# Kernel tuning notes

Measured on AMD Instinct MI355X. Metric: run time of the kernel, lower is better.

The kernel has to match this reference:

```python
import jax, jax.numpy as jnp
import numpy as np

R = 2
TAU = 0.1
EPS = 1e-7

# normalized 3x3 Sobel kernels (kornia SpatialGradient, normalized=True -> /8)
_GX = jnp.array([[-1., 0., 1.], [-2., 0., 2.], [-1., 0., 1.]], dtype=jnp.float32) / 8.0
_GY = _GX.T

K = 2 * R - 1  # 3
_HORIZ = jnp.zeros((K, K), jnp.float32).at[R - 1, :].set(1.0)
_VERT = jnp.zeros((K, K), jnp.float32).at[:, R - 1].set(1.0)
_LEAD = jnp.eye(K, dtype=jnp.float32)
_CNT = jnp.fliplr(jnp.eye(K, dtype=jnp.float32))


def _conv2d_same(x, k2d, mode):
    # depthwise 'same' cross-correlation, x: (B,C,H,W), k2d: (k,k)
    C = x.shape[1]
    p = k2d.shape[-1] // 2
    xp = jnp.pad(x, ((0, 0), (0, 0), (p, p), (p, p)), mode=mode)
    kern = jnp.broadcast_to(k2d[None, None], (C, 1) + k2d.shape)
    return jax.lax.conv_general_dilated(
        xp, kern, (1, 1), 'VALID',
        dimension_numbers=('NCHW', 'OIHW', 'NCHW'),
        feature_group_count=C)


def _grad_angles(t):
    # kornia SpatialGradient pads with replicate ('edge')
    gx = _conv2d_same(t, _GX, 'edge')
    gy = _conv2d_same(t, _GY, 'edge')
    grad_xx = _conv2d_same(gx, _GX, 'edge')
    grad_xy = _conv2d_same(gy, _GX, 'edge')
    grad_yy = _conv2d_same(gy, _GY, 'edge')
    theta = jnp.arctan(grad_yy * jnp.sign(-grad_xy + EPS) / (grad_xx + EPS))
    angle = theta * (180.0 / np.pi)
    return jnp.where(angle < 0, angle + 180.0, angle)


def _nms_loss(true_labels, pred_labels):
    angle = _grad_angles(true_labels)
    mask = (true_labels > 0).astype(jnp.float32)

    th_h = mask * (((angle >= 0) & (angle < 22.5)) | ((angle >= 157.5) & (angle < 180))).astype(jnp.float32)
    th_cd = mask * ((angle >= 22.5) & (angle < 67.5)).astype(jnp.float32)
    th_v = mask * ((angle >= 67.5) & (angle < 112.5)).astype(jnp.float32)
    th_ld = mask * ((angle > 112.5) & (angle < 157.5)).astype(jnp.float32)

    e = jnp.exp(pred_labels * TAU)

    def term(th, kern):
        f = _conv2d_same(e, kern, 'reflect')  # kornia filter2D default border 'reflect'
        return th * jnp.log(jnp.clip(e / (f + EPS), EPS, 1.0))

    total = (term(th_h, _HORIZ) + term(th_v, _VERT) +
             term(th_ld, _LEAD) + term(th_cd, _CNT))
    # sum over (C,H,W) per sample, mean over batch, negate
    return -jnp.mean(jnp.sum(total, axis=(1, 2, 3)))


def setup_inputs() -> dict:
    key = jax.random.key(0)
    k1, k2 = jax.random.split(key)
    B, C, H, W = 4, 19, 512, 512
    true_labels = jax.random.normal(k1, (B, C, H, W), dtype=jnp.float32)
    pred_labels = jax.random.normal(k2, (B, C, H, W), dtype=jnp.float32)
    return {"true_labels": true_labels, "pred_labels": pred_labels}


def reference(true_labels, pred_labels):
    return _nms_loss(true_labels, pred_labels)
```

## Files before the change

### kernel.cpp

```cpp
#include <hip/hip_runtime.h>

#define BAND 16
#define NITER (BAND + 4)
#define NSLOT 1024

__global__ __launch_bounds__(64) void nms_loss_kernel(
    const float* __restrict__ tl, const float* __restrict__ pl,
    double* __restrict__ acc_d, float* __restrict__ acc_f,
    int H, int W)
{
    const int y0   = blockIdx.x * BAND;
    const int slab = blockIdx.y;
    const int ch   = blockIdx.z;
    const float* tc = tl + (size_t)ch * H * W;
    const float* pc = pl + (size_t)ch * H * W;
    const int tid  = threadIdx.x;
    const int c0 = (slab << 7) + (tid << 1);
    const int oa = min(max(c0 - 2, 0), W - 2);
    const int oc = min(c0 + 2, W - 2);
    const bool xedge = (c0 == 0) || (c0 == W - 2);

    float P1h[5][2], P2h[5][2], P3h[5][2];
    float eh[3][4], tch[3][2];
    float tA[6], pA[6], tB[6], pB[6];

    #define LOADROW(I, T6, P6) {                                                   \
        int tr_ = y0 - 2 + (I); tr_ = min(max(tr_, 0), H - 1);                      \
        int pr_ = y0 - 3 + (I); pr_ = pr_ < 0 ? -pr_ : (pr_ >= H ? 2*H-2-pr_ : pr_);\
        const float* tb_ = tc + (size_t)tr_ * W;                                    \
        const float* pb_ = pc + (size_t)pr_ * W;                                    \
        float2 a_ = *(const float2*)(tb_ + oa), b_ = *(const float2*)(tb_ + c0),    \
               c_ = *(const float2*)(tb_ + oc);                                     \
        T6[0]=a_.x; T6[1]=a_.y; T6[2]=b_.x; T6[3]=b_.y; T6[4]=c_.x; T6[5]=c_.y;     \
        a_ = *(const float2*)(pb_ + oa); b_ = *(const float2*)(pb_ + c0);           \
        c_ = *(const float2*)(pb_ + oc);                                            \
        P6[0]=a_.x; P6[1]=a_.y; P6[2]=b_.x; P6[3]=b_.y; P6[4]=c_.x; P6[5]=c_.y; }

    #define CONSUME(T6, P6) {                                                       \
        if (!xedge) {                                                               \
            float s04 = T6[0] + T6[4], s13 = T6[1] + T6[3];                         \
            P1h[sP][0] = fmaf(-2.f, T6[2], s04);                                    \
            P3h[sP][0] = fmaf(6.f, T6[2], fmaf(4.f, s13, s04));                     \
            P2h[sP][0] = fmaf(2.f, T6[3] - T6[1], T6[4] - T6[0]);                   \
            float s04b = T6[1] + T6[5], s13b = T6[2] + T6[4];                       \
            P1h[sP][1] = fmaf(-2.f, T6[3], s04b);                                   \
            P3h[sP][1] = fmaf(6.f, T6[3], fmaf(4.f, s13b, s04b));                   \
            P2h[sP][1] = fmaf(2.f, T6[4] - T6[2], T6[5] - T6[1]);                   \
        } else if (c0 == 0) {                                                       \
            P1h[sP][0] = T6[4] - T6[3];                                             \
            P2h[sP][0] = fmaf(-2.f, T6[2], T6[3] + T6[4]);                          \
            P3h[sP][0] = fmaf(10.f, T6[2], fmaf(5.f, T6[3], T6[4]));                \
            P1h[sP][1] = fmaf(-2.f, T6[3], T6[2] + T6[5]);                          \
            P2h[sP][1] = fmaf(-3.f, T6[2], fmaf(2.f, T6[4], T6[5]));                \
            P3h[sP][1] = fmaf(5.f, T6[2], fmaf(6.f, T6[3], fmaf(4.f, T6[4], T6[5])));\
        } else {                                                                    \
            P1h[sP][0] = fmaf(-2.f, T6[2], T6[0] + T6[3]);                          \
            P2h[sP][0] = fmaf(3.f, T6[3], fmaf(-2.f, T6[1], -T6[0]));               \
            P3h[sP][0] = fmaf(5.f, T6[3], fmaf(6.f, T6[2], fmaf(4.f, T6[1], T6[0])));\
            P1h[sP][1] = T6[1] - T6[2];                                             \
            P2h[sP][1] = fmaf(2.f, T6[3], -T6[1] - T6[2]);                          \
            P3h[sP][1] = fmaf(10.f, T6[3], fmaf(5.f, T6[2], T6[1]));                \
        }                                                                           \
        tch[sE][0] = T6[2]; tch[sE][1] = T6[3];                                     \
        eh[sE][0] = __expf(0.1f * P6[1]);                                           \
        eh[sE][1] = __expf(0.1f * P6[2]);                                           \
        eh[sE][2] = __expf(0.1f * P6[3]);                                           \
        eh[sE][3] = __expf(0.1f * P6[4]); }

    LOADROW(0, tA, pA)
    LOADROW(1, tB, pB)

    float partial = 0.f;

    #pragma unroll
    for (int i = 0; i < NITER; ++i) {
        const int sP = i % 5, sE = i % 3;

        if ((i & 1) == 0) {
            CONSUME(tA, pA)
            if (i + 2 < NITER) LOADROW(i + 2, tA, pA)
        } else {
            CONSUME(tB, pB)
            if (i + 2 < NITER) LOADROW(i + 2, tB, pB)
        }

        if (i >= 4) {
            const int y = y0 + i - 4;
            const int s0 = (i - 4) % 5, s1 = (i - 3) % 5, s2 = (i - 2) % 5,
                      s3 = (i - 1) % 5, s4 = i % 5;
            float xx[2], xy[2], yy[2];
            if (y >= 2 && y <= H - 3) {
                #pragma unroll
                for (int j = 0; j < 2; ++j) {
                    float a04 = P1h[s0][j] + P1h[s4][j], a13 = P1h[s1][j] + P1h[s3][j];
                    xx[j] = fmaf(6.f, P1h[s2][j], fmaf(4.f, a13, a04));
                    xy[j] = fmaf(2.f, P2h[s3][j] - P2h[s1][j], P2h[s4][j] - P2h[s0][j]);
                    yy[j] = fmaf(-2.f, P3h[s2][j], P3h[s0][j] + P3h[s4][j]);
                }
            } else {
                float wss[5], wsd[5], wdd[5];
                if (y == 0) {
                    wss[0]=0; wss[1]=0; wss[2]=10; wss[3]=5;  wss[4]=1;
                    wsd[0]=0; wsd[1]=0; wsd[2]=-4; wsd[3]=3;  wsd[4]=1;
                    wdd[0]=0; wdd[1]=0; wdd[2]=0;  wdd[3]=-1; wdd[4]=1;
                } else if (y == 1) {
                    wss[0]=0; wss[1]=5; wss[2]=6;  wss[3]=4;  wss[4]=1;
                    wsd[0]=0; wsd[1]=-3;wsd[2]=0;  wsd[3]=2;  wsd[4]=1;
                    wdd[0]=0; wdd[1]=1; wdd[2]=-2; wdd[3]=0;  wdd[4]=1;
                } else if (y == H - 1) {
                    wss[0]=1; wss[1]=5; wss[2]=10; wss[3]=0;  wss[4]=0;
                    wsd[0]=-1;wsd[1]=-3;wsd[2]=4;  wsd[3]=0;  wsd[4]=0;
                    wdd[0]=1; wdd[1]=-1;wdd[2]=0;  wdd[3]=0;  wdd[4]=0;
                } else {
                    wss[0]=1; wss[1]=4; wss[2]=6;  wss[3]=5;  wss[4]=0;
                    wsd[0]=-1;wsd[1]=-2;wsd[2]=0;  wsd[3]=3;  wsd[4]=0;
                    wdd[0]=1; wdd[1]=0; wdd[2]=-2; wdd[3]=1;  wdd[4]=0;
                }
                const int ss[5] = {s0, s1, s2, s3, s4};
                #pragma unroll
                for (int j = 0; j < 2; ++j) {
                    float X = 0.f, Y = 0.f, Z = 0.f;
                    #pragma unroll
                    for (int k = 0; k < 5; ++k) {
                        X = fmaf(wss[k], P1h[ss[k]][j], X);
                        Y = fmaf(wsd[k], P2h[ss[k]][j], Y);
                        Z = fmaf(wdd[k], P3h[ss[k]][j], Z);
                    }
                    xx[j] = X; xy[j] = Y; yy[j] = Z;
                }
            }

            const int et = (i - 2) % 3, em = (i - 1) % 3, eb = i % 3;
            #pragma unroll
            for (int j = 0; j < 2; ++j) {
                if (tch[et][j] > 0.f) {
                    float den = xx[j] + 6.4e-6f;
                    float sa  = 6.4e-6f - xy[j];
                    float ax = fabsf(den), ay = fabsf(yy[j]);
                    bool isH = ay < 0.41421356f * ax;
                    bool isV = ay >= 2.41421356f * ax;
                    bool qp  = ((yy[j] * sa) * den) > 0.f;
                    float ec = eh[em][j + 1];
                    float n1 = isH ? eh[em][j + 2] : (isV ? eh[eb][j + 1] : (qp ? eh[eb][j] : eh[eb][j + 2]));
                    float n2 = isH ? eh[em][j]     : (isV ? eh[et][j + 1] : (qp ? eh[et][j + 2] : eh[et][j]));
                    partial += __logf(__fdividef(ec, ec + n1 + n2 + 1e-7f));
                }
            }
        }
    }

    for (int off = 32; off > 0; off >>= 1)
        partial += __shfl_down(partial, off, 64);
    if (tid == 0) {
        int fid = (blockIdx.z * gridDim.y + blockIdx.y) * gridDim.x + blockIdx.x;
        if (acc_d) atomicAdd(&acc_d[fid & (NSLOT - 1)], (double)partial);
        else       atomicAdd(acc_f, partial);
    }
}

__global__ void finalize_kernel(const double* acc_d, float* out,
                                int use_double, float inv_b)
{
    if (use_double) {
        int l = threadIdx.x;
        double s = 0.0;
        for (int i = l; i < NSLOT; i += 64) s += acc_d[i];
        for (int off = 32; off > 0; off >>= 1) s += __shfl_down(s, off, 64);
        if (l == 0) out[0] = (float)(-s * (double)inv_b);
    } else {
        if (threadIdx.x == 0) out[0] = -out[0] * inv_b;
    }
}

extern "C" void kernel_launch(void* const* d_in, const int* in_sizes, int n_in,
                              void* d_out, int out_size, void* d_ws, size_t ws_size,
                              hipStream_t stream)
{
    const float* tl = (const float*)d_in[0];
    const float* pl = (const float*)d_in[1];
    float* out = (float*)d_out;

    const int H = 512, W = 512, B = 4;

    double* acc_d = nullptr;
    float* acc_f = nullptr;
    int use_double = 0;
    if (ws_size >= NSLOT * sizeof(double)) {
        acc_d = (double*)d_ws;
        use_double = 1;
        hipMemsetAsync(acc_d, 0, NSLOT * sizeof(double), stream);
    } else {
        acc_f = out;
        hipMemsetAsync(out, 0, sizeof(float), stream);
    }

    dim3 grid(H / BAND, W / 128, 76);
    nms_loss_kernel<<<grid, 64, 0, stream>>>(tl, pl, acc_d, acc_f, H, W);
    finalize_kernel<<<1, 64, 0, stream>>>(acc_d, out, use_double, 1.0f / (float)B);
}
```

Measured before the change: 59.95 us.

## Process four columns per thread with float4 loads and branchless edge handling

Each thread now covers four columns instead of two, loading float4 vectors, and the grid's slab count is halved. The three-way x-edge branch and the y-edge weight tables are replaced by a uniform stencil plus small corrective terms using replicate/reflect substitution. Double-buffered prefetch two rows ahead is reduced to a single row ahead. The aim is to cut halo loads and redundant exp work per output and remove divergent edge code, at the cost of higher register use, half as many blocks, and a shallower prefetch.

```diff
diff --git a/kernel.cpp b/kernel.cpp
--- a/kernel.cpp
+++ b/kernel.cpp
@@ -14,61 +14,42 @@
     const int ch   = blockIdx.z;
     const float* tc = tl + (size_t)ch * H * W;
     const float* pc = pl + (size_t)ch * H * W;
-    const int tid  = threadIdx.x;
-    const int c0 = (slab << 7) + (tid << 1);
-    const int oa = min(max(c0 - 2, 0), W - 2);
-    const int oc = min(c0 + 2, W - 2);
-    const bool xedge = (c0 == 0) || (c0 == W - 2);
+    const int tid = threadIdx.x;
+    const int c0  = (slab << 8) + (tid << 2);
+    const int oa  = max(c0 - 4, 0);
+    const int oc  = min(c0 + 4, W - 4);
+    const bool eL = (c0 == 0), eR = (c0 == W - 4);
+    const float eL2 = eL ? 2.f : 0.f, eR2 = eR ? 2.f : 0.f;
 
-    float P1h[5][2], P2h[5][2], P3h[5][2];
-    float eh[3][4], tch[3][2];
-    float tA[6], pA[6], tB[6], pB[6];
+    float P1h[5][4], P2h[5][4], P3h[5][4];
+    float eh[3][6], tch[3][4];
+    float t12[12], p12[12];
 
-    #define LOADROW(I, T6, P6) {                                                   \
-        int tr_ = y0 - 2 + (I); tr_ = min(max(tr_, 0), H - 1);                      \
-        int pr_ = y0 - 3 + (I); pr_ = pr_ < 0 ? -pr_ : (pr_ >= H ? 2*H-2-pr_ : pr_);\
-        const float* tb_ = tc + (size_t)tr_ * W;                                    \
-        const float* pb_ = pc + (size_t)pr_ * W;                                    \
-        float2 a_ = *(const float2*)(tb_ + oa), b_ = *(const float2*)(tb_ + c0),    \
-               c_ = *(const float2*)(tb_ + oc);                                     \
-        T6[0]=a_.x; T6[1]=a_.y; T6[2]=b_.x; T6[3]=b_.y; T6[4]=c_.x; T6[5]=c_.y;     \
-        a_ = *(const float2*)(pb_ + oa); b_ = *(const float2*)(pb_ + c0);           \
-        c_ = *(const float2*)(pb_ + oc);                                            \
-        P6[0]=a_.x; P6[1]=a_.y; P6[2]=b_.x; P6[3]=b_.y; P6[4]=c_.x; P6[5]=c_.y; }
+    #define LOADROW(I) {                                                            \
+        int tr_ = y0 - 2 + (I); tr_ = min(max(tr_, 0), H - 1);                       \
+        int pr_ = y0 - 3 + (I); pr_ = pr_ < 0 ? -pr_ : (pr_ >= H ? 2*H-2-pr_ : pr_); \
+        const float* tb_ = tc + (size_t)tr_ * W;                                     \
+        const float* pb_ = pc + (size_t)pr_ * W;                                     \
+        float4 a_ = *(const float4*)(tb_ + oa);                                      \
+        float4 b_ = *(const float4*)(tb_ + c0);                                      \
+        float4 c_ = *(const float4*)(tb_ + oc);                                      \
+        t12[2]=a_.z; t12[3]=a_.w;                                                    \
+        t12[4]=b_.x; t12[5]=b_.y; t12[6]=b_.z; t12[7]=b_.w;                          \
+        t12[8]=c_.x; t12[9]=c_.y;                                                    \
+        a_ = *(const float4*)(pb_ + oa);                                             \
+        b_ = *(const float4*)(pb_ + c0);                                             \
+        c_ = *(const float4*)(pb_ + oc);                                             \
+        p12[3]=a_.w;                                                                 \
+        p12[4]=b_.x; p12[5]=b_.y; p12[6]=b_.z; p12[7]=b_.w;                          \
+        p12[8]=c_.x;                                                                 \
+        t12[2] = eL ? t12[5] : t12[2];                             \
+        t12[3] = eL ? t12[4] : t12[3];                             \
+        t12[8] = eR ? t12[7] : t12[8];                        \
+        t12[9] = eR ? t12[6] : t12[9];                        \
+        p12[3] = eL ? p12[5] : p12[3];                      \
+        p12[8] = eR ? p12[6] : p12[8]; }
 
-    #define CONSUME(T6, P6) {                                                       \
-        if (!xedge) {                                                               \
-            float s04 = T6[0] + T6[4], s13 = T6[1] + T6[3];                         \
-            P1h[sP][0] = fmaf(-2.f, T6[2], s04);                                    \
-            P3h[sP][0] = fmaf(6.f, T6[2], fmaf(4.f, s13, s04));                     \
-            P2h[sP][0] = fmaf(2.f, T6[3] - T6[1], T6[4] - T6[0]);                   \
-            float s04b = T6[1] + T6[5], s13b = T6[2] + T6[4];                       \
-            P1h[sP][1] = fmaf(-2.f, T6[3], s04b);                                   \
-            P3h[sP][1] = fmaf(6.f, T6[3], fmaf(4.f, s13b, s04b));                   \
-            P2h[sP][1] = fmaf(2.f, T6[4] - T6[2], T6[5] - T6[1]);                   \
-        } else if (c0 == 0) {                                                       \
-            P1h[sP][0] = T6[4] - T6[3];                                             \
-            P2h[sP][0] = fmaf(-2.f, T6[2], T6[3] + T6[4]);                          \
-            P3h[sP][0] = fmaf(10.f, T6[2], fmaf(5.f, T6[3], T6[4]));                \
-            P1h[sP][1] = fmaf(-2.f, T6[3], T6[2] + T6[5]);                          \
-            P2h[sP][1] = fmaf(-3.f, T6[2], fmaf(2.f, T6[4], T6[5]));                \
-            P3h[sP][1] = fmaf(5.f, T6[2], fmaf(6.f, T6[3], fmaf(4.f, T6[4], T6[5])));\
-        } else {                                                                    \
-            P1h[sP][0] = fmaf(-2.f, T6[2], T6[0] + T6[3]);                          \
-            P2h[sP][0] = fmaf(3.f, T6[3], fmaf(-2.f, T6[1], -T6[0]));               \
-            P3h[sP][0] = fmaf(5.f, T6[3], fmaf(6.f, T6[2], fmaf(4.f, T6[1], T6[0])));\
-            P1h[sP][1] = T6[1] - T6[2];                                             \
-            P2h[sP][1] = fmaf(2.f, T6[3], -T6[1] - T6[2]);                          \
-            P3h[sP][1] = fmaf(10.f, T6[3], fmaf(5.f, T6[2], T6[1]));                \
-        }                                                                           \
-        tch[sE][0] = T6[2]; tch[sE][1] = T6[3];                                     \
-        eh[sE][0] = __expf(0.1f * P6[1]);                                           \
-        eh[sE][1] = __expf(0.1f * P6[2]);                                           \
-        eh[sE][2] = __expf(0.1f * P6[3]);                                           \
-        eh[sE][3] = __expf(0.1f * P6[4]); }
-
-    LOADROW(0, tA, pA)
-    LOADROW(1, tB, pB)
+    LOADROW(0)
 
     float partial = 0.f;
 
@@ -76,70 +57,49 @@
     for (int i = 0; i < NITER; ++i) {
         const int sP = i % 5, sE = i % 3;
 
-        if ((i & 1) == 0) {
-            CONSUME(tA, pA)
-            if (i + 2 < NITER) LOADROW(i + 2, tA, pA)
-        } else {
-            CONSUME(tB, pB)
-            if (i + 2 < NITER) LOADROW(i + 2, tB, pB)
+        #pragma unroll
+        for (int j = 0; j < 4; ++j) {
+            float a0 = t12[j+2], a1 = t12[j+3], a2 = t12[j+4], a3 = t12[j+5], a4 = t12[j+6];
+            float s04 = a0 + a4, s13 = a1 + a3;
+            P1h[sP][j] = fmaf(-2.f, a2, s04);
+            P3h[sP][j] = fmaf(6.f, a2, fmaf(4.f, s13, s04));
+            P2h[sP][j] = fmaf(2.f, a3 - a1, a4 - a0);
+            tch[sE][j] = a2;
         }
+        P1h[sP][0] = fmaf(eL2, t12[4] - t12[5], P1h[sP][0]);
+        P1h[sP][3] = fmaf(eR2, t12[7] - t12[6], P1h[sP][3]);
+        #pragma unroll
+        for (int m = 0; m < 6; ++m) eh[sE][m] = __expf(0.1f * p12[m+3]);
+
+        if (i + 1 < NITER) LOADROW(i + 1)
 
         if (i >= 4) {
             const int y = y0 + i - 4;
-            const int s0 = (i - 4) % 5, s1 = (i - 3) % 5, s2 = (i - 2) % 5,
-                      s3 = (i - 1) % 5, s4 = i % 5;
-            float xx[2], xy[2], yy[2];
-            if (y >= 2 && y <= H - 3) {
-                #pragma unroll
-                for (int j = 0; j < 2; ++j) {
-                    float a04 = P1h[s0][j] + P1h[s4][j], a13 = P1h[s1][j] + P1h[s3][j];
-                    xx[j] = fmaf(6.f, P1h[s2][j], fmaf(4.f, a13, a04));
-                    xy[j] = fmaf(2.f, P2h[s3][j] - P2h[s1][j], P2h[s4][j] - P2h[s0][j]);
-                    yy[j] = fmaf(-2.f, P3h[s2][j], P3h[s0][j] + P3h[s4][j]);
+            const int s0=(i-4)%5, s1=(i-3)%5, s2=(i-2)%5, s3=(i-1)%5, s4=i%5;
+            const int et=(i-2)%3, em=(i-1)%3, eb=i%3;
+            const bool ytop = (y == 0), ybot = (y == H - 1);
+            #pragma unroll
+            for (int j = 0; j < 4; ++j) {
+                float a04 = P1h[s0][j] + P1h[s4][j], a13 = P1h[s1][j] + P1h[s3][j];
+                float xx = fmaf(6.f, P1h[s2][j], fmaf(4.f, a13, a04));
+                float xy = fmaf(2.f, P2h[s3][j] - P2h[s1][j], P2h[s4][j] - P2h[s0][j]);
+                float yy = fmaf(-2.f, P3h[s2][j], P3h[s0][j] + P3h[s4][j]);
+                if (ytop) {
+                    xx += P1h[s3][j] - P1h[s2][j];
+                    xy += P2h[s3][j] - P2h[s2][j];
+                    yy += P3h[s2][j] - P3h[s3][j];
+                } else if (ybot) {
+                    xx += P1h[s1][j] - P1h[s2][j];
+                    xy += P2h[s2][j] - P2h[s1][j];
+                    yy += P3h[s2][j] - P3h[s1][j];
                 }
-            } else {
-                float wss[5], wsd[5], wdd[5];
-                if (y == 0) {
-                    wss[0]=0; wss[1]=0; wss[2]=10; wss[3]=5;  wss[4]=1;
-                    wsd[0]=0; wsd[1]=0; wsd[2]=-4; wsd[3]=3;  wsd[4]=1;
-                    wdd[0]=0; wdd[1]=0; wdd[2]=0;  wdd[3]=-1; wdd[4]=1;
-                } else if (y == 1) {
-                    wss[0]=0; wss[1]=5; wss[2]=6;  wss[3]=4;  wss[4]=1;
-                    wsd[0]=0; wsd[1]=-3;wsd[2]=0;  wsd[3]=2;  wsd[4]=1;
-                    wdd[0]=0; wdd[1]=1; wdd[2]=-2; wdd[3]=0;  wdd[4]=1;
-                } else if (y == H - 1) {
-                    wss[0]=1; wss[1]=5; wss[2]=10; wss[3]=0;  wss[4]=0;
-                    wsd[0]=-1;wsd[1]=-3;wsd[2]=4;  wsd[3]=0;  wsd[4]=0;
-                    wdd[0]=1; wdd[1]=-1;wdd[2]=0;  wdd[3]=0;  wdd[4]=0;
-                } else {
-                    wss[0]=1; wss[1]=4; wss[2]=6;  wss[3]=5;  wss[4]=0;
-                    wsd[0]=-1;wsd[1]=-2;wsd[2]=0;  wsd[3]=3;  wsd[4]=0;
-                    wdd[0]=1; wdd[1]=0; wdd[2]=-2; wdd[3]=1;  wdd[4]=0;
-                }
-                const int ss[5] = {s0, s1, s2, s3, s4};
-                #pragma unroll
-                for (int j = 0; j < 2; ++j) {
-                    float X = 0.f, Y = 0.f, Z = 0.f;
-                    #pragma unroll
-                    for (int k = 0; k < 5; ++k) {
-                        X = fmaf(wss[k], P1h[ss[k]][j], X);
-                        Y = fmaf(wsd[k], P2h[ss[k]][j], Y);
-                        Z = fmaf(wdd[k], P3h[ss[k]][j], Z);
-                    }
-                    xx[j] = X; xy[j] = Y; yy[j] = Z;
-                }
-            }
-
-            const int et = (i - 2) % 3, em = (i - 1) % 3, eb = i % 3;
-            #pragma unroll
-            for (int j = 0; j < 2; ++j) {
                 if (tch[et][j] > 0.f) {
-                    float den = xx[j] + 6.4e-6f;
-                    float sa  = 6.4e-6f - xy[j];
-                    float ax = fabsf(den), ay = fabsf(yy[j]);
+                    float den = xx + 6.4e-6f;
+                    float sa  = 6.4e-6f - xy;
+                    float ax = fabsf(den), ay = fabsf(yy);
                     bool isH = ay < 0.41421356f * ax;
                     bool isV = ay >= 2.41421356f * ax;
-                    bool qp  = ((yy[j] * sa) * den) > 0.f;
+                    bool qp  = ((yy * sa) * den) > 0.f;
                     float ec = eh[em][j + 1];
                     float n1 = isH ? eh[em][j + 2] : (isV ? eh[eb][j + 1] : (qp ? eh[eb][j] : eh[eb][j + 2]));
                     float n2 = isH ? eh[em][j]     : (isV ? eh[et][j + 1] : (qp ? eh[et][j + 2] : eh[et][j]));
@@ -194,7 +154,7 @@
         hipMemsetAsync(out, 0, sizeof(float), stream);
     }
 
-    dim3 grid(H / BAND, W / 128, 76);
+    dim3 grid(H / BAND, W / 256, 76);
     nms_loss_kernel<<<grid, 64, 0, stream>>>(tl, pl, acc_d, acc_f, H, W);
     finalize_kernel<<<1, 64, 0, stream>>>(acc_d, out, use_double, 1.0f / (float)B);
 }
```

After: 60.56 us. About the same (+1.0%).
